# Performance work log

Hardware: AMD Instinct MI355X
Metric: run time of the kernel (lower is better)

Reference implementation:

```python
import jax, jax.numpy as jnp
import numpy as np

B = 1024        # batch of clips
MAX_LEN = 14    # temporal length, pinned by spatial_shapes=[[max_len,1]]
D_MODEL = 1024
N_HEADS = 16
N_POINTS = 4
H_SP, W_SP = MAX_LEN, 1  # level-0 spatial shape (H, W)


def setup_inputs() -> dict:
    key = jax.random.key(0)
    ks = jax.random.split(key, 12)
    s = 0.02
    lin = lambda k, i, o: (jax.random.normal(k, (i, o), jnp.float32) * s)
    vec = lambda k, o: (jax.random.normal(k, (o,), jnp.float32) * s)
    return {
        "x": jax.random.normal(ks[0], (B, MAX_LEN, D_MODEL), jnp.float32),
        "W_value": lin(ks[1], D_MODEL, D_MODEL), "b_value": vec(ks[2], D_MODEL),
        "W_off": lin(ks[3], D_MODEL, N_HEADS * N_POINTS * 2), "b_off": vec(ks[4], N_HEADS * N_POINTS * 2),
        "W_attn": lin(ks[5], D_MODEL, N_HEADS * N_POINTS), "b_attn": vec(ks[6], N_HEADS * N_POINTS),
        "W_out": lin(ks[7], D_MODEL, D_MODEL), "b_out": vec(ks[8], D_MODEL),
        "W_proj": lin(ks[9], D_MODEL, D_MODEL), "b_proj": vec(ks[10], D_MODEL),
    }


def _msdeform(x, W_value, b_value, W_off, b_off, W_attn, b_attn, W_out, b_out):
    Bq, T, D = x.shape
    heads, P = N_HEADS, N_POINTS
    hd = D // heads
    # value projection -> [B, heads, N=H*W, hd]
    value = (x @ W_value + b_value).reshape(Bq, T, heads, hd).transpose(0, 2, 1, 3)
    # sampling offsets [B,T,heads,P,2] and softmax attention weights [B,T,heads,P]
    off = (x @ W_off + b_off).reshape(Bq, T, heads, P, 2)
    aw = jax.nn.softmax((x @ W_attn + b_attn).reshape(Bq, T, heads, P), axis=-1)
    # reference points: x-coord = linspace(0,1,T), y-coord = 0
    ref = jnp.linspace(0.0, 1.0, T, dtype=x.dtype)
    ref_pts = jnp.stack([ref, jnp.zeros_like(ref)], axis=-1)  # [T,2]
    norm = jnp.array([W_SP, H_SP], dtype=x.dtype)  # offset_normalizer = (W, H)
    locs = ref_pts[None, :, None, None, :] + off / norm  # [B,T,heads,P,2] in [0,1] coords
    # grid_sample bilinear, align_corners=False, padding_mode='zeros':
    # pixel coord = loc * size - 0.5
    ix = locs[..., 0] * W_SP - 0.5
    iy = locs[..., 1] * H_SP - 0.5
    x0 = jnp.floor(ix); y0 = jnp.floor(iy)
    fx = ix - x0; fy = iy - y0
    x0i = x0.astype(jnp.int32); y0i = y0.astype(jnp.int32)
    out = jnp.zeros((Bq, heads, T * P, hd), x.dtype)
    corners = ((0, 0, (1 - fx) * (1 - fy)), (1, 0, fx * (1 - fy)),
               (0, 1, (1 - fx) * fy), (1, 1, fx * fy))
    for dx, dy, w in corners:
        xx = x0i + dx; yy = y0i + dy
        valid = ((xx >= 0) & (xx < W_SP) & (yy >= 0) & (yy < H_SP)).astype(x.dtype)
        idx = jnp.clip(yy, 0, H_SP - 1) * W_SP + jnp.clip(xx, 0, W_SP - 1)  # [B,T,heads,P]
        idx_t = idx.transpose(0, 2, 1, 3).reshape(Bq, heads, T * P)
        v = jnp.take_along_axis(value, idx_t[..., None], axis=2)  # [B,heads,T*P,hd]
        wt = (w * valid).transpose(0, 2, 1, 3).reshape(Bq, heads, T * P)
        out = out + v * wt[..., None]
    out = out.reshape(Bq, heads, T, P, hd)
    attn = jnp.einsum('bhqpd,bqhp->bqhd', out, aw).reshape(Bq, T, D)
    return attn @ W_out + b_out


def reference(x, W_value, b_value, W_off, b_off, W_attn, b_attn, W_out, b_out, W_proj, b_proj):
    y = _msdeform(x, W_value, b_value, W_off, b_off, W_attn, b_attn, W_out, b_out)
    return y @ W_proj + b_proj
```

## Files before the change

kernel.cpp:

```cpp
#include <hip/hip_runtime.h>
#include <hip/hip_bf16.h>

using bf16 = __hip_bfloat16;
typedef __attribute__((ext_vector_type(8))) short bf16x8;
typedef __attribute__((ext_vector_type(4))) float f32x4;

#define NB   1024
#define TT   14
#define DM   1024
#define ROWS (NB*TT)
#define NCAT 1280

__device__ __forceinline__ unsigned short f2b(float f) {
  union { bf16 h; unsigned short u; } cv; cv.h = __float2bfloat16(f); return cv.u;
}

__device__ __forceinline__ void gload16(const bf16* g, bf16* l) {
  __builtin_amdgcn_global_load_lds((const __attribute__((address_space(1))) void*)g,
                                   (__attribute__((address_space(3))) void*)l, 16, 0, 0);
}

__global__ __launch_bounds__(256) void k_conv_bf16(const float* __restrict__ in,
                                                   bf16* __restrict__ out, int n4) {
  int idx = blockIdx.x * 256 + threadIdx.x;
  int stride = gridDim.x * 256;
  for (int i = idx; i < n4; i += stride) {
    float4 v = reinterpret_cast<const float4*>(in)[i];
    ushort4 o;
    o.x = f2b(v.x); o.y = f2b(v.y); o.z = f2b(v.z); o.w = f2b(v.w);
    reinterpret_cast<ushort4*>(out)[i] = o;
  }
}

__global__ __launch_bounds__(256) void k_transpose(const float* __restrict__ in,
                                                   bf16* __restrict__ out, int Nin) {
  __shared__ float t[32][33];
  int k0 = blockIdx.x * 32, n0 = blockIdx.y * 32;
  int lx = threadIdx.x & 31, ly = threadIdx.x >> 5;
#pragma unroll
  for (int r = 0; r < 32; r += 8)
    t[ly + r][lx] = in[(size_t)(k0 + ly + r) * Nin + (n0 + lx)];
  __syncthreads();
#pragma unroll
  for (int r = 0; r < 32; r += 8)
    out[(size_t)(n0 + ly + r) * 1024 + (k0 + lx)] = __float2bfloat16(t[lx][ly + r]);
}

__global__ __launch_bounds__(256) void k_prep_wcat(const float* __restrict__ Wv,
                                                   const float* __restrict__ Wo,
                                                   const float* __restrict__ Wa,
                                                   bf16* __restrict__ out) {
  __shared__ float t[32][33];
  int k0 = blockIdx.x * 32, n0 = blockIdx.y * 32;
  int lx = threadIdx.x & 31, ly = threadIdx.x >> 5;
  const float* src; int base, width;
  if (n0 < 1024)      { src = Wv; base = 0;    width = 1024; }
  else if (n0 < 1152) { src = Wo; base = 1024; width = 128;  }
  else if (n0 < 1216) { src = Wa; base = 1152; width = 64;   }
  else                { src = nullptr; base = 0; width = 1;  }
#pragma unroll
  for (int r = 0; r < 32; r += 8)
    t[ly + r][lx] = src ? src[(size_t)(k0 + ly + r) * width + (n0 - base + lx)] : 0.0f;
  __syncthreads();
#pragma unroll
  for (int r = 0; r < 32; r += 8)
    out[(size_t)(n0 + ly + r) * 1024 + (k0 + lx)] = __float2bfloat16(t[lx][ly + r]);
}

__global__ __launch_bounds__(256) void k_bcat(const float* bv, const float* bo,
                                              const float* ba, float* out) {
  int i = blockIdx.x * 256 + threadIdx.x;
  if (i >= NCAT) return;
  float v = 0.0f;
  if (i < 1024) v = bv[i];
  else if (i < 1152) v = bo[i - 1024];
  else if (i < 1216) v = ba[i - 1152];
  out[i] = v;
}

__global__ __launch_bounds__(256) void k_bcomb(const float* __restrict__ b_out,
                                               const float* __restrict__ W_proj,
                                               const float* __restrict__ b_proj,
                                               float* __restrict__ out) {
  __shared__ float part[4][64];
  int j0 = blockIdx.x * 64;
  int jl = threadIdx.x & 63, ip = threadIdx.x >> 6;
  int j = j0 + jl;
  float acc = 0.0f;
  int i0 = ip * 256;
  for (int i = i0; i < i0 + 256; ++i)
    acc = fmaf(b_out[i], W_proj[(size_t)i * 1024 + j], acc);
  part[ip][jl] = acc;
  __syncthreads();
  if (threadIdx.x < 64) {
    int jj = j0 + threadIdx.x;
    out[jj] = part[0][threadIdx.x] + part[1][threadIdx.x] +
              part[2][threadIdx.x] + part[3][threadIdx.x] + b_proj[jj];
  }
}

template<int OUT_BF16, int HAS_BIAS, int SWZ>
__global__ __launch_bounds__(256, 4) void k_gemm_bt(const bf16* __restrict__ A,
                                                    const bf16* __restrict__ Bt,
                                                    void* __restrict__ Cv,
                                                    const float* __restrict__ bias,
                                                    int M, int N, int K,
                                                    int lda, int ldb) {
  __shared__ bf16 As[2 * 4096];
  __shared__ bf16 Bs[2 * 4096];
  const int tid  = threadIdx.x;
  const int wave = tid >> 6, lane = tid & 63;

  int bid = blockIdx.y * gridDim.x + blockIdx.x;
  if (SWZ) {
    int nwg = gridDim.x * gridDim.y;
    int q = nwg >> 3, r = nwg & 7;
    int xcd = bid & 7, li = bid >> 3;
    bid = (xcd < r ? xcd * (q + 1) : r * (q + 1) + (xcd - r) * q) + li;
  }
  const int bx = bid % gridDim.x, by = bid / gridDim.x;
  const int row0 = by * 128, col0 = bx * 128;
  const int wr = (wave >> 1) * 64, wc = (wave & 1) * 64;
  f32x4 acc[4][4] = {};

  const int sr = tid >> 2;
  const int sc = (tid & 3) * 8;
  const bf16* Ab  = A  + (size_t)(row0 + sr) * lda + sc;
  const bf16* Ab2 = Ab + (size_t)64 * lda;
  const bf16* Bb  = Bt + (size_t)(col0 + sr) * ldb + sc;
  const bf16* Bb2 = Bb + (size_t)64 * ldb;

  const int fr = lane & 15;
  const int kb = (lane >> 4) * 8;
  const int nk = K >> 5;

  auto STAGE = [&](int buf, int kk) {
    const int ko = kk * 32;
    bf16* asd = As + buf * 4096 + tid * 8;
    bf16* bsd = Bs + buf * 4096 + tid * 8;
    gload16(Ab  + ko, asd);
    gload16(Ab2 + ko, asd + 2048);
    gload16(Bb  + ko, bsd);
    gload16(Bb2 + ko, bsd + 2048);
  };
  auto COMPUTE = [&](int buf) {
    const bf16* as = As + buf * 4096;
    const bf16* bs = Bs + buf * 4096;
    bf16x8 af[4], bfr[4];
#pragma unroll
    for (int mi = 0; mi < 4; ++mi)
      af[mi] = *(const bf16x8*)(as + (wr + mi * 16 + fr) * 32 + kb);
#pragma unroll
    for (int ni = 0; ni < 4; ++ni)
      bfr[ni] = *(const bf16x8*)(bs + (wc + ni * 16 + fr) * 32 + kb);
#pragma unroll
    for (int mi = 0; mi < 4; ++mi)
#pragma unroll
      for (int ni = 0; ni < 4; ++ni)
        acc[mi][ni] = __builtin_amdgcn_mfma_f32_16x16x32_bf16(af[mi], bfr[ni], acc[mi][ni], 0, 0, 0);
  };

  STAGE(0, 0);
  asm volatile("s_waitcnt vmcnt(0)" ::: "memory");
  __syncthreads();
  int cur = 0;
  for (int kk = 1; kk < nk; ++kk) {
    STAGE(cur ^ 1, kk);
    COMPUTE(cur);
    asm volatile("s_waitcnt vmcnt(0)" ::: "memory");
    __syncthreads();
    cur ^= 1;
  }
  COMPUTE(cur);

  const int fq = (lane >> 4) * 4;
#pragma unroll
  for (int mi = 0; mi < 4; ++mi) {
#pragma unroll
    for (int ni = 0; ni < 4; ++ni) {
      int gr = row0 + wr + mi * 16 + fq;
      int gc = col0 + wc + ni * 16 + fr;
      float bv = HAS_BIAS ? bias[gc] : 0.0f;
#pragma unroll
      for (int r = 0; r < 4; ++r) {
        float v = acc[mi][ni][r] + bv;
        if (OUT_BF16) ((bf16*)Cv)[(size_t)(gr + r) * N + gc] = __float2bfloat16(v);
        else          ((float*)Cv)[(size_t)(gr + r) * N + gc] = v;
      }
    }
  }
}

__global__ __launch_bounds__(256) void k_sample(const bf16* __restrict__ C1,
                                                bf16* __restrict__ y) {
  const int wave = threadIdx.x >> 6, lane = threadIdx.x & 63;
  const int row = blockIdx.x * 4 + wave;
  const int b = row / TT, t = row - b * TT;
  const bf16* r1 = C1 + (size_t)row * NCAT;

  float offx, offy;
  {
    ushort2 u = *reinterpret_cast<const ushort2*>(r1 + 1024 + lane * 2);
    offx = __uint_as_float(((unsigned)u.x) << 16);
    offy = __uint_as_float(((unsigned)u.y) << 16);
  }
  float logit;
  {
    unsigned short u = reinterpret_cast<const unsigned short*>(r1)[1152 + lane];
    logit = __uint_as_float(((unsigned)u) << 16);
  }
  float m = fmaxf(logit, __shfl_xor(logit, 1));
  m = fmaxf(m, __shfl_xor(m, 2));
  float e = __expf(logit - m);
  float s = e + __shfl_xor(e, 1);
  s = s + __shfl_xor(s, 2);
  float aw = e / s;

  const float refx = (float)t * (1.0f / 13.0f);
  float ix = refx + offx - 0.5f;
  float xf = floorf(ix);
  float fx = ix - xf;
  float wx = (xf == 0.0f) ? (1.0f - fx) : ((xf == -1.0f) ? fx : 0.0f);

  float iy = offy - 0.5f;
  float yf = floorf(iy);
  float fy = iy - yf;
  int y0 = (int)yf, y1 = y0 + 1;
  float w0 = (y0 >= 0 && y0 < TT) ? (1.0f - fy) : 0.0f;
  float w1 = (y1 >= 0 && y1 < TT) ? fy : 0.0f;
  int i0 = max(0, min(TT - 1, y0));
  int i1 = max(0, min(TT - 1, y1));
  float cw0 = aw * wx * w0;
  float cw1 = aw * wx * w1;

  const bf16* vb = C1 + (size_t)(b * TT) * NCAT;
  float acc[16];
#pragma unroll
  for (int h = 0; h < 16; ++h) acc[h] = 0.0f;
#pragma unroll
  for (int j = 0; j < 64; ++j) {
    float c0 = __shfl(cw0, j);
    float c1 = __shfl(cw1, j);
    int a0 = __shfl(i0, j);
    int a1 = __shfl(i1, j);
    const int hh = j >> 2;
    float v0 = __bfloat162float(vb[(size_t)a0 * NCAT + hh * 64 + lane]);
    float v1 = __bfloat162float(vb[(size_t)a1 * NCAT + hh * 64 + lane]);
    acc[hh] = fmaf(c0, v0, fmaf(c1, v1, acc[hh]));
  }
#pragma unroll
  for (int h = 0; h < 16; ++h)
    y[(size_t)row * DM + h * 64 + lane] = __float2bfloat16(acc[h]);
}

extern "C" void kernel_launch(void* const* d_in, const int* in_sizes, int n_in,
                              void* d_out, int out_size, void* d_ws, size_t ws_size,
                              hipStream_t stream) {
  (void)in_sizes; (void)n_in; (void)out_size; (void)ws_size;
  const float* x       = (const float*)d_in[0];
  const float* W_value = (const float*)d_in[1];
  const float* b_value = (const float*)d_in[2];
  const float* W_off   = (const float*)d_in[3];
  const float* b_off   = (const float*)d_in[4];
  const float* W_attn  = (const float*)d_in[5];
  const float* b_attn  = (const float*)d_in[6];
  const float* W_out   = (const float*)d_in[7];
  const float* b_out   = (const float*)d_in[8];
  const float* W_proj  = (const float*)d_in[9];
  const float* b_proj  = (const float*)d_in[10];

  char* ws = (char*)d_ws;
  bf16*  x_bf    = (bf16*)(ws);
  bf16*  y_bf    = x_bf;
  bf16*  C1      = (bf16*)(ws + 29360128);
  bf16*  Wcat_t  = (bf16*)(ws + 66060288);
  float* bcat    = (float*)(ws + 68681728);
  bf16*  Wout_b  = (bf16*)(ws + 68686848);
  bf16*  Wproj_t = (bf16*)(ws + 70784000);
  bf16*  Wc_t    = (bf16*)(ws + 72881152);
  float* bcomb   = (float*)(ws + 74978304);

  k_conv_bf16<<<2048, 256, 0, stream>>>(x, x_bf, ROWS * DM / 4);
  k_prep_wcat<<<dim3(32, 40), 256, 0, stream>>>(W_value, W_off, W_attn, Wcat_t);
  k_bcat<<<5, 256, 0, stream>>>(b_value, b_off, b_attn, bcat);
  k_conv_bf16<<<256, 256, 0, stream>>>(W_out, Wout_b, 1024 * 1024 / 4);
  k_transpose<<<dim3(32, 32), 256, 0, stream>>>(W_proj, Wproj_t, 1024);
  k_bcomb<<<16, 256, 0, stream>>>(b_out, W_proj, b_proj, bcomb);

  k_gemm_bt<1, 0, 0><<<dim3(8, 8), 256, 0, stream>>>(
      Wproj_t, Wout_b, Wc_t, nullptr, 1024, 1024, 1024, 1024, 1024);

  k_gemm_bt<1, 1, 1><<<dim3(NCAT / 128, ROWS / 128), 256, 0, stream>>>(
      x_bf, Wcat_t, C1, bcat, ROWS, NCAT, DM, DM, DM);

  k_sample<<<ROWS / 4, 256, 0, stream>>>(C1, y_bf);

  k_gemm_bt<0, 1, 1><<<dim3(DM / 128, ROWS / 128), 256, 0, stream>>>(
      y_bf, Wc_t, (float*)d_out, bcomb, ROWS, DM, DM, DM, DM);
}
```

Measured before the change: 195.4 us.

## Triple-buffer GEMM LDS pipeline with swizzled layout and vectorized epilogue

Reworks the bf16 MFMA GEMM into a three-stage LDS pipeline. Loads for tile k+2 are issued while tile k is computed, and a partial vmcnt wait replaces the full drain each iteration. The LDS layout gets an XOR swizzle to cut bank conflicts, MFMA operands are swapped so each lane holds 4 consecutive columns, and the epilogue writes float4/ushort4 vectors with vector bias loads. Tile size is now a template parameter and the small weight-combine GEMM uses 64x64 tiles. s_setprio is added around the MFMA block. The extra LDS stage lowers occupancy from 4 to 3 blocks per CU.

```diff
diff --git a/kernel.cpp b/kernel.cpp
--- a/kernel.cpp
+++ b/kernel.cpp
@@ -99,15 +99,22 @@
   }
 }
 
-template<int OUT_BF16, int HAS_BIAS, int SWZ>
-__global__ __launch_bounds__(256, 4) void k_gemm_bt(const bf16* __restrict__ A,
+template<int BM, int BN, int OUT_BF16, int HAS_BIAS, int SWZ>
+__global__ __launch_bounds__(256, 3) void k_gemm_bt(const bf16* __restrict__ A,
                                                     const bf16* __restrict__ Bt,
                                                     void* __restrict__ Cv,
                                                     const float* __restrict__ bias,
-                                                    int M, int N, int K,
+                                                    int N, int K,
                                                     int lda, int ldb) {
-  __shared__ bf16 As[2 * 4096];
-  __shared__ bf16 Bs[2 * 4096];
+  constexpr int LA  = BM / 64;
+  constexpr int LB  = BN / 64;
+  constexpr int ASZ = BM * 32;
+  constexpr int BSZ = BN * 32;
+  constexpr int MR  = BM / 32;
+  constexpr int NR  = BN / 32;
+  __shared__ bf16 As[3 * ASZ];
+  __shared__ bf16 Bs[3 * BSZ];
+
   const int tid  = threadIdx.x;
   const int wave = tid >> 6, lane = tid & 63;
 
@@ -119,73 +126,91 @@
     bid = (xcd < r ? xcd * (q + 1) : r * (q + 1) + (xcd - r) * q) + li;
   }
   const int bx = bid % gridDim.x, by = bid / gridDim.x;
-  const int row0 = by * 128, col0 = bx * 128;
-  const int wr = (wave >> 1) * 64, wc = (wave & 1) * 64;
-  f32x4 acc[4][4] = {};
-
-  const int sr = tid >> 2;
-  const int sc = (tid & 3) * 8;
-  const bf16* Ab  = A  + (size_t)(row0 + sr) * lda + sc;
-  const bf16* Ab2 = Ab + (size_t)64 * lda;
-  const bf16* Bb  = Bt + (size_t)(col0 + sr) * ldb + sc;
-  const bf16* Bb2 = Bb + (size_t)64 * ldb;
-
-  const int fr = lane & 15;
-  const int kb = (lane >> 4) * 8;
+  const int row0 = by * BM, col0 = bx * BN;
+  const int wr = (wave >> 1) * (BM / 2), wc = (wave & 1) * (BN / 2);
+  f32x4 acc[MR][NR] = {};
+
+  const int sr  = tid >> 2;
+  const int scb = (tid & 3) ^ ((sr + (sr >> 2)) & 3);
+  const bf16* Ab = A  + (size_t)(row0 + sr) * lda + scb * 8;
+  const bf16* Bb = Bt + (size_t)(col0 + sr) * ldb + scb * 8;
+
+  const int fr = lane & 15, g = lane >> 4;
+  int aoff[MR], boff[NR];
+#pragma unroll
+  for (int mi = 0; mi < MR; ++mi) {
+    int row = wr + mi * 16 + fr, h = row >> 6, lr = row & 63;
+    aoff[mi] = h * 2048 + (lr * 4 + (g ^ ((lr + (lr >> 2)) & 3))) * 8;
+  }
+#pragma unroll
+  for (int ni = 0; ni < NR; ++ni) {
+    int row = wc + ni * 16 + fr, h = row >> 6, lr = row & 63;
+    boff[ni] = h * 2048 + (lr * 4 + (g ^ ((lr + (lr >> 2)) & 3))) * 8;
+  }
+
+  auto STAGE = [&](int s, int kk) {
+    const int ko = kk * 32;
+#pragma unroll
+    for (int j = 0; j < LA; ++j)
+      gload16(Ab + (size_t)j * 64 * lda + ko, As + s * ASZ + j * 2048 + tid * 8);
+#pragma unroll
+    for (int j = 0; j < LB; ++j)
+      gload16(Bb + (size_t)j * 64 * ldb + ko, Bs + s * BSZ + j * 2048 + tid * 8);
+  };
+  auto COMPUTE = [&](int s) {
+    const bf16* as = As + s * ASZ;
+    const bf16* bs = Bs + s * BSZ;
+    bf16x8 af[MR], bfm[NR];
+#pragma unroll
+    for (int mi = 0; mi < MR; ++mi) af[mi] = *(const bf16x8*)(as + aoff[mi]);
+#pragma unroll
+    for (int ni = 0; ni < NR; ++ni) bfm[ni] = *(const bf16x8*)(bs + boff[ni]);
+    __builtin_amdgcn_s_setprio(1);
+#pragma unroll
+    for (int mi = 0; mi < MR; ++mi)
+#pragma unroll
+      for (int ni = 0; ni < NR; ++ni)
+        acc[mi][ni] = __builtin_amdgcn_mfma_f32_16x16x32_bf16(bfm[ni], af[mi], acc[mi][ni], 0, 0, 0);
+    __builtin_amdgcn_s_setprio(0);
+  };
+
   const int nk = K >> 5;
-
-  auto STAGE = [&](int buf, int kk) {
-    const int ko = kk * 32;
-    bf16* asd = As + buf * 4096 + tid * 8;
-    bf16* bsd = Bs + buf * 4096 + tid * 8;
-    gload16(Ab  + ko, asd);
-    gload16(Ab2 + ko, asd + 2048);
-    gload16(Bb  + ko, bsd);
-    gload16(Bb2 + ko, bsd + 2048);
-  };
-  auto COMPUTE = [&](int buf) {
-    const bf16* as = As + buf * 4096;
-    const bf16* bs = Bs + buf * 4096;
-    bf16x8 af[4], bfr[4];
-#pragma unroll
-    for (int mi = 0; mi < 4; ++mi)
-      af[mi] = *(const bf16x8*)(as + (wr + mi * 16 + fr) * 32 + kb);
-#pragma unroll
-    for (int ni = 0; ni < 4; ++ni)
-      bfr[ni] = *(const bf16x8*)(bs + (wc + ni * 16 + fr) * 32 + kb);
-#pragma unroll
-    for (int mi = 0; mi < 4; ++mi)
-#pragma unroll
-      for (int ni = 0; ni < 4; ++ni)
-        acc[mi][ni] = __builtin_amdgcn_mfma_f32_16x16x32_bf16(af[mi], bfr[ni], acc[mi][ni], 0, 0, 0);
-  };
-
   STAGE(0, 0);
-  asm volatile("s_waitcnt vmcnt(0)" ::: "memory");
-  __syncthreads();
+  STAGE(1, 1);
   int cur = 0;
-  for (int kk = 1; kk < nk; ++kk) {
-    STAGE(cur ^ 1, kk);
+  for (int i = 0; i < nk; ++i) {
+    if (i < nk - 1) asm volatile("s_waitcnt vmcnt(%0)" :: "i"(LA + LB) : "memory");
+    else            asm volatile("s_waitcnt vmcnt(0)" ::: "memory");
+    __builtin_amdgcn_s_barrier();
+    asm volatile("" ::: "memory");
+    if (i + 2 < nk) {
+      int s2 = cur + 2; if (s2 >= 3) s2 -= 3;
+      STAGE(s2, i + 2);
+    }
     COMPUTE(cur);
-    asm volatile("s_waitcnt vmcnt(0)" ::: "memory");
-    __syncthreads();
-    cur ^= 1;
-  }
-  COMPUTE(cur);
-
-  const int fq = (lane >> 4) * 4;
-#pragma unroll
-  for (int mi = 0; mi < 4; ++mi) {
-#pragma unroll
-    for (int ni = 0; ni < 4; ++ni) {
-      int gr = row0 + wr + mi * 16 + fq;
-      int gc = col0 + wc + ni * 16 + fr;
-      float bv = HAS_BIAS ? bias[gc] : 0.0f;
-#pragma unroll
-      for (int r = 0; r < 4; ++r) {
-        float v = acc[mi][ni][r] + bv;
-        if (OUT_BF16) ((bf16*)Cv)[(size_t)(gr + r) * N + gc] = __float2bfloat16(v);
-        else          ((float*)Cv)[(size_t)(gr + r) * N + gc] = v;
+    if (++cur == 3) cur = 0;
+  }
+
+  const int fq = g * 4;
+#pragma unroll
+  for (int mi = 0; mi < MR; ++mi) {
+    int gr = row0 + wr + mi * 16 + fr;
+#pragma unroll
+    for (int ni = 0; ni < NR; ++ni) {
+      int gc = col0 + wc + ni * 16 + fq;
+      float b0 = 0, b1 = 0, b2 = 0, b3 = 0;
+      if (HAS_BIAS) {
+        float4 bv = *reinterpret_cast<const float4*>(bias + gc);
+        b0 = bv.x; b1 = bv.y; b2 = bv.z; b3 = bv.w;
+      }
+      float v0 = acc[mi][ni][0] + b0, v1 = acc[mi][ni][1] + b1;
+      float v2 = acc[mi][ni][2] + b2, v3 = acc[mi][ni][3] + b3;
+      if (OUT_BF16) {
+        ushort4 u; u.x = f2b(v0); u.y = f2b(v1); u.z = f2b(v2); u.w = f2b(v3);
+        *reinterpret_cast<ushort4*>((bf16*)Cv + (size_t)gr * N + gc) = u;
+      } else {
+        float4 o; o.x = v0; o.y = v1; o.z = v2; o.w = v3;
+        *reinterpret_cast<float4*>((float*)Cv + (size_t)gr * N + gc) = o;
       }
     }
   }
@@ -287,14 +312,14 @@
   k_transpose<<<dim3(32, 32), 256, 0, stream>>>(W_proj, Wproj_t, 1024);
   k_bcomb<<<16, 256, 0, stream>>>(b_out, W_proj, b_proj, bcomb);
 
-  k_gemm_bt<1, 0, 0><<<dim3(8, 8), 256, 0, stream>>>(
-      Wproj_t, Wout_b, Wc_t, nullptr, 1024, 1024, 1024, 1024, 1024);
-
-  k_gemm_bt<1, 1, 1><<<dim3(NCAT / 128, ROWS / 128), 256, 0, stream>>>(
-      x_bf, Wcat_t, C1, bcat, ROWS, NCAT, DM, DM, DM);
+  k_gemm_bt<64, 64, 1, 0, 0><<<dim3(16, 16), 256, 0, stream>>>(
+      Wproj_t, Wout_b, Wc_t, nullptr, 1024, 1024, 1024, 1024);
+
+  k_gemm_bt<128, 128, 1, 1, 1><<<dim3(NCAT / 128, ROWS / 128), 256, 0, stream>>>(
+      x_bf, Wcat_t, C1, bcat, NCAT, DM, DM, DM);
 
   k_sample<<<ROWS / 4, 256, 0, stream>>>(C1, y_bf);
 
-  k_gemm_bt<0, 1, 1><<<dim3(DM / 128, ROWS / 128), 256, 0, stream>>>(
-      y_bf, Wc_t, (float*)d_out, bcomb, ROWS, DM, DM, DM, DM);
-}
+  k_gemm_bt<128, 128, 0, 1, 1><<<dim3(DM / 128, ROWS / 128), 256, 0, stream>>>(
+      y_bf, Wc_t, (float*)d_out, bcomb, DM, DM, DM, DM);
+}
```

After: 203.8 us. 4.3% more time.
